# Kernel optimization log

Measured on AMD Instinct MI355X. Metric: run time of the kernel, lower is better.

Reference implementation:

```python
import jax, jax.numpy as jnp
import numpy as np
from jax.scipy.special import logsumexp

EPSILON = 0.1
MAX_ITERS = 20

B, S, T = 8, 2048, 2048


def setup_inputs() -> dict:
    key = jax.random.key(0)
    k1, k2, k3 = jax.random.split(key, 3)
    cost = jax.random.normal(k1, (B, S, T), dtype=jnp.float32)
    mu = jax.random.uniform(k2, (B, S), dtype=jnp.float32)
    nu = jax.random.uniform(k3, (B, T), dtype=jnp.float32)
    # normalize to probability distributions (realistic OT marginals)
    mu = mu / jnp.sum(mu, axis=-1, keepdims=True)
    nu = nu / jnp.sum(nu, axis=-1, keepdims=True)
    return {"cost": cost, "mu": mu, "nu": nu}


def reference(cost, mu, nu):
    tiny = jnp.finfo(cost.dtype).tiny
    log_mu = jnp.log(jnp.maximum(mu, tiny))          # (B, S)
    log_nu = jnp.log(jnp.maximum(nu, tiny))          # (B, T)
    log_K = -cost / EPSILON                          # (B, S, T)

    def step(carry, _):
        log_u, log_v = carry
        # row update: logsumexp over targets
        log_u = log_mu - logsumexp(log_K + log_v[:, None, :], axis=-1)  # (B, S)
        # col update: logsumexp over sources (equiv. to transpose in torch code)
        log_v = log_nu - logsumexp(log_K + log_u[:, :, None], axis=-2)  # (B, T)
        return (log_u, log_v), None

    init = (jnp.zeros_like(log_mu), jnp.zeros_like(log_nu))
    (log_u, log_v), _ = jax.lax.scan(step, init, None, length=MAX_ITERS)

    log_pi = log_u[:, :, None] + log_K + log_v[:, None, :]  # (B, S, T)
    transport = jnp.exp(log_pi)
    return transport, log_pi
```

## Files before the change

kernel.cpp:

```cpp
#include <hip/hip_runtime.h>
#include <hip/hip_fp16.h>
#include <math.h>

#define BB 8
#define SS 2048
#define TT 2048
#define ITERS 20
#define NEG_EPS_INV -10.0f
#define ROWS 16
#define NCHUNK 2
#define NTILE (SS / ROWS)
#define TINYF 1.17549435e-38f

typedef float vfloat4 __attribute__((ext_vector_type(4)));

__device__ __forceinline__ float4 fma4v(float a, float4 x, float4 y) {
    return make_float4(fmaf(a, x.x, y.x), fmaf(a, x.y, y.y),
                       fmaf(a, x.z, y.z), fmaf(a, x.w, y.w));
}
__device__ __forceinline__ float4 max4(float4 a, float4 b) {
    return make_float4(fmaxf(a.x, b.x), fmaxf(a.y, b.y),
                       fmaxf(a.z, b.z), fmaxf(a.w, b.w));
}
__device__ __forceinline__ float hmax4(float4 a) {
    return fmaxf(fmaxf(a.x, a.y), fmaxf(a.z, a.w));
}
__device__ __forceinline__ float hsum4(float4 a) {
    return (a.x + a.y) + (a.z + a.w);
}
__device__ __forceinline__ float4 exp4m(float4 x, float m) {
    return make_float4(__expf(x.x - m), __expf(x.y - m),
                       __expf(x.z - m), __expf(x.w - m));
}
__device__ __forceinline__ uint h2u(__half2 h) {
    union { __half2 h; uint u; } c; c.h = h; return c.u;
}
__device__ __forceinline__ __half2 u2h(uint u) {
    union { __half2 h; uint u; } c; c.u = u; return c.h;
}
__device__ __forceinline__ uint2 pack4(float4 f) {
    uint2 r;
    r.x = h2u(__float22half2_rn(make_float2(f.x, f.y)));
    r.y = h2u(__float22half2_rn(make_float2(f.z, f.w)));
    return r;
}
__device__ __forceinline__ float4 unpack4(uint2 u) {
    float2 a = __half22float2(u2h(u.x));
    float2 b = __half22float2(u2h(u.y));
    return make_float4(a.x, a.y, b.x, b.y);
}
__device__ __forceinline__ void nt_store4(float4 v, float* p) {
    vfloat4 x = {v.x, v.y, v.z, v.w};
    __builtin_nontemporal_store(x, reinterpret_cast<vfloat4*>(p));
}

__global__ __launch_bounds__(256) void init_logv(float* __restrict__ log_v) {
    log_v[blockIdx.x * 256 + threadIdx.x] = 0.0f;
}

template <bool FIRST>
__global__ __launch_bounds__(256, 3) void fused_pass(
        const float* __restrict__ cost, const uint2* __restrict__ c16r,
        uint2* __restrict__ c16w, const float* __restrict__ mu,
        const float* __restrict__ log_v, float* __restrict__ log_u,
        float* __restrict__ P) {
    int t = threadIdx.x;
    int w = t >> 6, l = t & 63;
    int tile = blockIdx.x, b = blockIdx.y;

    __shared__ float4 lds[4][512];

    const float4* v4 = (const float4*)(log_v + (size_t)b * TT);
    float4 vv[8];
#pragma unroll
    for (int i = 0; i < 8; ++i) vv[i] = v4[i * 64 + l];

#pragma unroll
    for (int i = 0; i < 8; ++i) lds[w][i * 64 + l] = make_float4(0.f, 0.f, 0.f, 0.f);

#pragma unroll
    for (int c = 0; c < NCHUNK; ++c) {
        int r0 = tile * ROWS + c * 8 + w * 2;
        size_t rowbase = (size_t)(b * SS + r0) * TT;

        float4 x0[8], x1[8];
        if constexpr (FIRST) {
            const float4* c4 = (const float4*)(cost + rowbase);
            uint2* cw = c16w + rowbase / 4;
#pragma unroll
            for (int i = 0; i < 8; ++i) x0[i] = c4[i * 64 + l];
#pragma unroll
            for (int i = 0; i < 8; ++i) x1[i] = c4[512 + i * 64 + l];
#pragma unroll
            for (int i = 0; i < 8; ++i) {
                cw[i * 64 + l] = pack4(x0[i]);
                cw[512 + i * 64 + l] = pack4(x1[i]);
            }
        } else {
            const uint2* cr = c16r + rowbase / 4;
#pragma unroll
            for (int i = 0; i < 8; ++i) x0[i] = unpack4(cr[i * 64 + l]);
#pragma unroll
            for (int i = 0; i < 8; ++i) x1[i] = unpack4(cr[512 + i * 64 + l]);
        }
#pragma unroll
        for (int i = 0; i < 8; ++i) {
            x0[i] = fma4v(NEG_EPS_INV, x0[i], vv[i]);
            x1[i] = fma4v(NEG_EPS_INV, x1[i], vv[i]);
        }

        float4 a0 = x0[0], a1 = x1[0];
#pragma unroll
        for (int i = 1; i < 8; ++i) { a0 = max4(a0, x0[i]); a1 = max4(a1, x1[i]); }
        float m0 = hmax4(a0), m1 = hmax4(a1);
#pragma unroll
        for (int off = 1; off < 64; off <<= 1) {
            m0 = fmaxf(m0, __shfl_xor(m0, off));
            m1 = fmaxf(m1, __shfl_xor(m1, off));
        }

        float ps0 = 0.0f, ps1 = 0.0f;
#pragma unroll
        for (int i = 0; i < 8; ++i) {
            x0[i] = exp4m(x0[i], m0);
            x1[i] = exp4m(x1[i], m1);
            ps0 += hsum4(x0[i]);
            ps1 += hsum4(x1[i]);
        }
#pragma unroll
        for (int off = 1; off < 64; off <<= 1) {
            ps0 += __shfl_xor(ps0, off);
            ps1 += __shfl_xor(ps1, off);
        }

        float g0 = mu[b * SS + r0] / ps0;
        float g1 = mu[b * SS + r0 + 1] / ps1;
        if (l == 0) {
            log_u[b * SS + r0]     = __logf(fmaxf(g0, TINYF)) - m0;
            log_u[b * SS + r0 + 1] = __logf(fmaxf(g1, TINYF)) - m1;
        }

#pragma unroll
        for (int i = 0; i < 8; ++i) {
            float4 o = lds[w][i * 64 + l];
            o.x = fmaf(g0, x0[i].x, fmaf(g1, x1[i].x, o.x));
            o.y = fmaf(g0, x0[i].y, fmaf(g1, x1[i].y, o.y));
            o.z = fmaf(g0, x0[i].z, fmaf(g1, x1[i].z, o.z));
            o.w = fmaf(g0, x0[i].w, fmaf(g1, x1[i].w, o.w));
            lds[w][i * 64 + l] = o;
        }
    }
    __syncthreads();

    float4* P4 = (float4*)P + (size_t)(tile * BB + b) * 512;
#pragma unroll
    for (int k = 0; k < 2; ++k) {
        int j = k * 256 + t;
        float4 s0 = lds[0][j], s1 = lds[1][j], s2 = lds[2][j], s3 = lds[3][j];
        float4 o;
        o.x = (s0.x + s1.x) + (s2.x + s3.x);
        o.y = (s0.y + s1.y) + (s2.y + s3.y);
        o.z = (s0.z + s1.z) + (s2.z + s3.z);
        o.w = (s0.w + s1.w) + (s2.w + s3.w);
        P4[j] = o;
    }
}

__global__ __launch_bounds__(256) void combine_v(
        const float* __restrict__ P, const float* __restrict__ nu,
        float* __restrict__ log_v) {
    int t = threadIdx.x;
    int seg = t >> 6, ci = t & 63;
    int col = blockIdx.x * 64 + ci;
    int b = blockIdx.y;

    float s = 0.0f;
#pragma unroll 8
    for (int k = 0; k < NTILE / 4; ++k) {
        int tile = seg * (NTILE / 4) + k;
        s += P[((size_t)tile * BB + b) * TT + col];
    }
    __shared__ float lds[4][64];
    lds[seg][ci] = s;
    __syncthreads();
    if (t < 64) {
        float tot = (lds[0][ci] + lds[1][ci]) + (lds[2][ci] + lds[3][ci]);
        int i = b * TT + col;
        log_v[i] = __logf(fmaxf(nu[i], TINYF)) + log_v[i] - __logf(fmaxf(tot, TINYF));
    }
}

__global__ __launch_bounds__(256) void finalize(const uint2* __restrict__ c16,
                                                const float* __restrict__ log_u,
                                                const float* __restrict__ log_v,
                                                float* __restrict__ transport,
                                                float* __restrict__ log_pi) {
    int i = blockIdx.x * 256 + threadIdx.x;
    int flat = i * 4;
    int row = flat >> 11;
    int t = flat & (TT - 1);
    int b = row >> 11;

    float lu = log_u[row];
    float4 lv = *reinterpret_cast<const float4*>(log_v + (size_t)b * TT + t);
    float4 c = unpack4(c16[((size_t)row * TT + t) / 4]);

    float4 lp;
    lp.x = fmaf(NEG_EPS_INV, c.x, lu + lv.x);
    lp.y = fmaf(NEG_EPS_INV, c.y, lu + lv.y);
    lp.z = fmaf(NEG_EPS_INV, c.z, lu + lv.z);
    lp.w = fmaf(NEG_EPS_INV, c.w, lu + lv.w);

    float4 tr;
    tr.x = __expf(lp.x);
    tr.y = __expf(lp.y);
    tr.z = __expf(lp.z);
    tr.w = __expf(lp.w);

    nt_store4(tr, transport + (size_t)row * TT + t);
    nt_store4(lp, log_pi + (size_t)row * TT + t);
}

extern "C" void kernel_launch(void* const* d_in, const int* in_sizes, int n_in,
                              void* d_out, int out_size, void* d_ws, size_t ws_size,
                              hipStream_t stream) {
    const float* cost = (const float*)d_in[0];
    const float* mu = (const float*)d_in[1];
    const float* nu = (const float*)d_in[2];

    float* out = (float*)d_out;
    float* transport = out;
    float* log_pi = out + (size_t)BB * SS * TT;

    float* ws = (float*)d_ws;
    float* log_u = ws;
    float* log_v = ws + 16384;
    float* P = ws + (1 << 20);
    uint2* c16 = (uint2*)(ws + (1 << 23));

    hipLaunchKernelGGL(init_logv, dim3(BB * TT / 256), dim3(256), 0, stream, log_v);

    hipLaunchKernelGGL((fused_pass<true>), dim3(NTILE, BB), dim3(256), 0, stream,
                       cost, c16, c16, mu, log_v, log_u, P);
    hipLaunchKernelGGL(combine_v, dim3(TT / 64, BB), dim3(256), 0, stream,
                       P, nu, log_v);

    for (int it = 1; it < ITERS; ++it) {
        hipLaunchKernelGGL((fused_pass<false>), dim3(NTILE, BB), dim3(256), 0, stream,
                           cost, c16, c16, mu, log_v, log_u, P);
        hipLaunchKernelGGL(combine_v, dim3(TT / 64, BB), dim3(256), 0, stream,
                           P, nu, log_v);
    }

    hipLaunchKernelGGL(finalize, dim3(BB * SS * TT / 4 / 256), dim3(256), 0, stream,
                       c16, log_u, log_v, transport, log_pi);
}
```

Baseline: 509.1 us.

## Fuse all Sinkhorn iterations into one cooperative persistent kernel with grid syncs

```diff
diff --git a/kernel.cpp b/kernel.cpp
--- a/kernel.cpp
+++ b/kernel.cpp
@@ -1,14 +1,19 @@
 #include <hip/hip_runtime.h>
+#include <hip/hip_cooperative_groups.h>
 #include <hip/hip_fp16.h>
 #include <math.h>
+
+namespace cg = cooperative_groups;
 
 #define BB 8
 #define SS 2048
 #define TT 2048
 #define ITERS 20
 #define NEG_EPS_INV -10.0f
-#define ROWS 16
-#define NCHUNK 2
+#define NWAVE 8
+#define RPW 2
+#define NCHUNK 4
+#define ROWS (NWAVE * RPW * NCHUNK)
 #define NTILE (SS / ROWS)
 #define TINYF 1.17549435e-38f
 
@@ -54,139 +59,133 @@
     __builtin_nontemporal_store(x, reinterpret_cast<vfloat4*>(p));
 }
 
-__global__ __launch_bounds__(256) void init_logv(float* __restrict__ log_v) {
-    log_v[blockIdx.x * 256 + threadIdx.x] = 0.0f;
-}
-
-template <bool FIRST>
-__global__ __launch_bounds__(256, 3) void fused_pass(
-        const float* __restrict__ cost, const uint2* __restrict__ c16r,
-        uint2* __restrict__ c16w, const float* __restrict__ mu,
-        const float* __restrict__ log_v, float* __restrict__ log_u,
+__global__ __launch_bounds__(256) void init_logs(const float* __restrict__ nu,
+                                                 float* __restrict__ log_nu,
+                                                 float* __restrict__ log_v) {
+    int i = blockIdx.x * 256 + threadIdx.x;
+    log_nu[i] = __logf(fmaxf(nu[i], TINYF));
+    log_v[i] = 0.0f;
+}
+
+__global__ __launch_bounds__(512, 2) void sinkhorn_loop(
+        const float* __restrict__ cost, uint2* __restrict__ c16,
+        const float* __restrict__ mu, const float* __restrict__ log_nu,
+        float* __restrict__ log_u, float* __restrict__ log_v,
         float* __restrict__ P) {
+    cg::grid_group gg = cg::this_grid();
     int t = threadIdx.x;
     int w = t >> 6, l = t & 63;
-    int tile = blockIdx.x, b = blockIdx.y;
-
-    __shared__ float4 lds[4][512];
-
-    const float4* v4 = (const float4*)(log_v + (size_t)b * TT);
-    float4 vv[8];
-#pragma unroll
-    for (int i = 0; i < 8; ++i) vv[i] = v4[i * 64 + l];
-
-#pragma unroll
-    for (int i = 0; i < 8; ++i) lds[w][i * 64 + l] = make_float4(0.f, 0.f, 0.f, 0.f);
-
-#pragma unroll
-    for (int c = 0; c < NCHUNK; ++c) {
-        int r0 = tile * ROWS + c * 8 + w * 2;
-        size_t rowbase = (size_t)(b * SS + r0) * TT;
-
-        float4 x0[8], x1[8];
-        if constexpr (FIRST) {
-            const float4* c4 = (const float4*)(cost + rowbase);
-            uint2* cw = c16w + rowbase / 4;
-#pragma unroll
-            for (int i = 0; i < 8; ++i) x0[i] = c4[i * 64 + l];
-#pragma unroll
-            for (int i = 0; i < 8; ++i) x1[i] = c4[512 + i * 64 + l];
+    int bid = blockIdx.x;
+    int tile = bid & (NTILE - 1);
+    int b = bid >> 5;
+
+    __shared__ float4 lds[NWAVE][512];
+
+    for (int it = 0; it < ITERS; ++it) {
+        const float4* v4 = (const float4*)(log_v + (size_t)b * TT);
+        float4 vv[8];
+#pragma unroll
+        for (int i = 0; i < 8; ++i) vv[i] = v4[i * 64 + l];
+
+#pragma unroll
+        for (int i = 0; i < 8; ++i) lds[w][i * 64 + l] = make_float4(0.f, 0.f, 0.f, 0.f);
+
+#pragma unroll
+        for (int c = 0; c < NCHUNK; ++c) {
+            int r0 = tile * ROWS + c * (NWAVE * RPW) + w * RPW;
+            size_t rowbase = (size_t)(b * SS + r0) * TT;
+
+            float4 x0[8], x1[8];
+            if (it == 0) {
+                const float4* c4 = (const float4*)(cost + rowbase);
+                uint2* cw = c16 + rowbase / 4;
+#pragma unroll
+                for (int i = 0; i < 8; ++i) x0[i] = c4[i * 64 + l];
+#pragma unroll
+                for (int i = 0; i < 8; ++i) x1[i] = c4[512 + i * 64 + l];
+#pragma unroll
+                for (int i = 0; i < 8; ++i) {
+                    cw[i * 64 + l] = pack4(x0[i]);
+                    cw[512 + i * 64 + l] = pack4(x1[i]);
+                }
+            } else {
+                const uint2* cr = c16 + rowbase / 4;
+#pragma unroll
+                for (int i = 0; i < 8; ++i) x0[i] = unpack4(cr[i * 64 + l]);
+#pragma unroll
+                for (int i = 0; i < 8; ++i) x1[i] = unpack4(cr[512 + i * 64 + l]);
+            }
 #pragma unroll
             for (int i = 0; i < 8; ++i) {
-                cw[i * 64 + l] = pack4(x0[i]);
-                cw[512 + i * 64 + l] = pack4(x1[i]);
-            }
-        } else {
-            const uint2* cr = c16r + rowbase / 4;
-#pragma unroll
-            for (int i = 0; i < 8; ++i) x0[i] = unpack4(cr[i * 64 + l]);
-#pragma unroll
-            for (int i = 0; i < 8; ++i) x1[i] = unpack4(cr[512 + i * 64 + l]);
+                x0[i] = fma4v(NEG_EPS_INV, x0[i], vv[i]);
+                x1[i] = fma4v(NEG_EPS_INV, x1[i], vv[i]);
+            }
+
+            float4 a0 = x0[0], a1 = x1[0];
+#pragma unroll
+            for (int i = 1; i < 8; ++i) { a0 = max4(a0, x0[i]); a1 = max4(a1, x1[i]); }
+            float m0 = hmax4(a0), m1 = hmax4(a1);
+#pragma unroll
+            for (int off = 1; off < 64; off <<= 1) {
+                m0 = fmaxf(m0, __shfl_xor(m0, off));
+                m1 = fmaxf(m1, __shfl_xor(m1, off));
+            }
+
+            float ps0 = 0.0f, ps1 = 0.0f;
+#pragma unroll
+            for (int i = 0; i < 8; ++i) {
+                x0[i] = exp4m(x0[i], m0);
+                x1[i] = exp4m(x1[i], m1);
+                ps0 += hsum4(x0[i]);
+                ps1 += hsum4(x1[i]);
+            }
+#pragma unroll
+            for (int off = 1; off < 64; off <<= 1) {
+                ps0 += __shfl_xor(ps0, off);
+                ps1 += __shfl_xor(ps1, off);
+            }
+
+            float g0 = mu[b * SS + r0] / ps0;
+            float g1 = mu[b * SS + r0 + 1] / ps1;
+            if (l == 0) {
+                log_u[b * SS + r0]     = __logf(fmaxf(g0, TINYF)) - m0;
+                log_u[b * SS + r0 + 1] = __logf(fmaxf(g1, TINYF)) - m1;
+            }
+
+#pragma unroll
+            for (int i = 0; i < 8; ++i) {
+                float4 o = lds[w][i * 64 + l];
+                o.x = fmaf(g0, x0[i].x, fmaf(g1, x1[i].x, o.x));
+                o.y = fmaf(g0, x0[i].y, fmaf(g1, x1[i].y, o.y));
+                o.z = fmaf(g0, x0[i].z, fmaf(g1, x1[i].z, o.z));
+                o.w = fmaf(g0, x0[i].w, fmaf(g1, x1[i].w, o.w));
+                lds[w][i * 64 + l] = o;
+            }
         }
-#pragma unroll
-        for (int i = 0; i < 8; ++i) {
-            x0[i] = fma4v(NEG_EPS_INV, x0[i], vv[i]);
-            x1[i] = fma4v(NEG_EPS_INV, x1[i], vv[i]);
+        __syncthreads();
+
+        float4* P4 = (float4*)(P + ((size_t)(b * NTILE + tile)) * TT);
+        float4 s = lds[0][t];
+#pragma unroll
+        for (int w2 = 1; w2 < NWAVE; ++w2) {
+            float4 q = lds[w2][t];
+            s.x += q.x; s.y += q.y; s.z += q.z; s.w += q.w;
         }
-
-        float4 a0 = x0[0], a1 = x1[0];
-#pragma unroll
-        for (int i = 1; i < 8; ++i) { a0 = max4(a0, x0[i]); a1 = max4(a1, x1[i]); }
-        float m0 = hmax4(a0), m1 = hmax4(a1);
-#pragma unroll
-        for (int off = 1; off < 64; off <<= 1) {
-            m0 = fmaxf(m0, __shfl_xor(m0, off));
-            m1 = fmaxf(m1, __shfl_xor(m1, off));
+        P4[t] = s;
+
+        gg.sync();
+
+        int g = bid * 512 + t;
+        if (g < BB * TT) {
+            int gb = g >> 11, col = g & (TT - 1);
+            const float* Pc = P + (size_t)gb * NTILE * TT + col;
+            float tot = 0.0f;
+#pragma unroll 8
+            for (int t2 = 0; t2 < NTILE; ++t2) tot += Pc[(size_t)t2 * TT];
+            log_v[g] = log_nu[g] + log_v[g] - __logf(fmaxf(tot, TINYF));
         }
 
-        float ps0 = 0.0f, ps1 = 0.0f;
-#pragma unroll
-        for (int i = 0; i < 8; ++i) {
-            x0[i] = exp4m(x0[i], m0);
-            x1[i] = exp4m(x1[i], m1);
-            ps0 += hsum4(x0[i]);
-            ps1 += hsum4(x1[i]);
-        }
-#pragma unroll
-        for (int off = 1; off < 64; off <<= 1) {
-            ps0 += __shfl_xor(ps0, off);
-            ps1 += __shfl_xor(ps1, off);
-        }
-
-        float g0 = mu[b * SS + r0] / ps0;
-        float g1 = mu[b * SS + r0 + 1] / ps1;
-        if (l == 0) {
-            log_u[b * SS + r0]     = __logf(fmaxf(g0, TINYF)) - m0;
-            log_u[b * SS + r0 + 1] = __logf(fmaxf(g1, TINYF)) - m1;
-        }
-
-#pragma unroll
-        for (int i = 0; i < 8; ++i) {
-            float4 o = lds[w][i * 64 + l];
-            o.x = fmaf(g0, x0[i].x, fmaf(g1, x1[i].x, o.x));
-            o.y = fmaf(g0, x0[i].y, fmaf(g1, x1[i].y, o.y));
-            o.z = fmaf(g0, x0[i].z, fmaf(g1, x1[i].z, o.z));
-            o.w = fmaf(g0, x0[i].w, fmaf(g1, x1[i].w, o.w));
-            lds[w][i * 64 + l] = o;
-        }
-    }
-    __syncthreads();
-
-    float4* P4 = (float4*)P + (size_t)(tile * BB + b) * 512;
-#pragma unroll
-    for (int k = 0; k < 2; ++k) {
-        int j = k * 256 + t;
-        float4 s0 = lds[0][j], s1 = lds[1][j], s2 = lds[2][j], s3 = lds[3][j];
-        float4 o;
-        o.x = (s0.x + s1.x) + (s2.x + s3.x);
-        o.y = (s0.y + s1.y) + (s2.y + s3.y);
-        o.z = (s0.z + s1.z) + (s2.z + s3.z);
-        o.w = (s0.w + s1.w) + (s2.w + s3.w);
-        P4[j] = o;
-    }
-}
-
-__global__ __launch_bounds__(256) void combine_v(
-        const float* __restrict__ P, const float* __restrict__ nu,
-        float* __restrict__ log_v) {
-    int t = threadIdx.x;
-    int seg = t >> 6, ci = t & 63;
-    int col = blockIdx.x * 64 + ci;
-    int b = blockIdx.y;
-
-    float s = 0.0f;
-#pragma unroll 8
-    for (int k = 0; k < NTILE / 4; ++k) {
-        int tile = seg * (NTILE / 4) + k;
-        s += P[((size_t)tile * BB + b) * TT + col];
-    }
-    __shared__ float lds[4][64];
-    lds[seg][ci] = s;
-    __syncthreads();
-    if (t < 64) {
-        float tot = (lds[0][ci] + lds[1][ci]) + (lds[2][ci] + lds[3][ci]);
-        int i = b * TT + col;
-        log_v[i] = __logf(fmaxf(nu[i], TINYF)) + log_v[i] - __logf(fmaxf(tot, TINYF));
+        gg.sync();
     }
 }
 
@@ -235,22 +234,17 @@
     float* ws = (float*)d_ws;
     float* log_u = ws;
     float* log_v = ws + 16384;
+    float* log_nu = ws + 32768;
     float* P = ws + (1 << 20);
     uint2* c16 = (uint2*)(ws + (1 << 23));
 
-    hipLaunchKernelGGL(init_logv, dim3(BB * TT / 256), dim3(256), 0, stream, log_v);
-
-    hipLaunchKernelGGL((fused_pass<true>), dim3(NTILE, BB), dim3(256), 0, stream,
-                       cost, c16, c16, mu, log_v, log_u, P);
-    hipLaunchKernelGGL(combine_v, dim3(TT / 64, BB), dim3(256), 0, stream,
-                       P, nu, log_v);
-
-    for (int it = 1; it < ITERS; ++it) {
-        hipLaunchKernelGGL((fused_pass<false>), dim3(NTILE, BB), dim3(256), 0, stream,
-                           cost, c16, c16, mu, log_v, log_u, P);
-        hipLaunchKernelGGL(combine_v, dim3(TT / 64, BB), dim3(256), 0, stream,
-                           P, nu, log_v);
-    }
+    hipLaunchKernelGGL(init_logs, dim3(BB * TT / 256), dim3(256), 0, stream,
+                       nu, log_nu, log_v);
+
+    void* args[] = {(void*)&cost, (void*)&c16, (void*)&mu, (void*)&log_nu,
+                    (void*)&log_u, (void*)&log_v, (void*)&P};
+    hipLaunchCooperativeKernel(reinterpret_cast<void*>(sinkhorn_loop),
+                               dim3(NTILE * BB), dim3(512), args, 0, stream);
 
     hipLaunchKernelGGL(finalize, dim3(BB * SS * TT / 4 / 256), dim3(256), 0, stream,
                        c16, log_u, log_v, transport, log_pi);
```

New measurement: 1.613 ms. +216.8%, slower.
